# Kernel tuning notes

Measured on AMD Instinct MI355X. Metric: run time of the kernel, lower is better.

Reference implementation:

```python
import jax, jax.numpy as jnp
import numpy as np

B, S, D, H = 4, 1024, 1024, 16
DH = D // H


def setup_inputs() -> dict:
    key = jax.random.key(0)
    ks = jax.random.split(key, 9)
    s = 0.02
    return {
        "x": jax.random.normal(ks[0], (B, S, D), dtype=jnp.float32),
        "mask": jax.random.randint(ks[1], (B, 1, S), 0, 2, dtype=jnp.int32),
        "Wq": jax.random.normal(ks[2], (D, D), dtype=jnp.float32) * s,
        "bq": jnp.zeros((D,), dtype=jnp.float32),
        "Wk": jax.random.normal(ks[3], (D, D), dtype=jnp.float32) * s,
        "Wv": jax.random.normal(ks[4], (D, D), dtype=jnp.float32) * s,
        "bv": jnp.zeros((D,), dtype=jnp.float32),
        "Wo": jax.random.normal(ks[5], (D, D), dtype=jnp.float32) * s,
        "bo": jnp.zeros((D,), dtype=jnp.float32),
    }


def reference(x, mask, Wq, bq, Wk, Wv, bv, Wo, bo):
    # Linear projections (torch Linear: y = x @ W.T + b)
    q = x @ Wq.T + bq
    k = x @ Wk.T  # key has bias=False
    v = x @ Wv.T + bv

    scale = jnp.asarray(DH, x.dtype) ** (-0.25)
    # [B,S,D] -> [B,H,S,DH]
    qh = q.reshape(B, S, H, DH).transpose(0, 2, 1, 3) * scale
    kh = k.reshape(B, S, H, DH).transpose(0, 2, 1, 3) * scale
    vh = v.reshape(B, S, H, DH).transpose(0, 2, 1, 3)

    qk = jnp.einsum("bhqd,bhkd->bhqk", qh, kh)  # [B,H,S,S]

    # pad-mask branch: mask [B,1,S] -> [B,1,1,S], 0 means padded
    pad = (mask == 0)[:, :, None, :]
    min_value = jnp.finfo(qk.dtype).min
    qk = jnp.where(pad, min_value, qk)

    qk = qk.astype(jnp.float32)
    w = jax.nn.softmax(qk, axis=-1).astype(x.dtype)
    w = jnp.where(pad, jnp.asarray(0.0, w.dtype), w)

    wv = jnp.einsum("bhqk,bhkd->bhqd", w, vh)  # [B,H,S,DH]
    wv = wv.transpose(0, 2, 1, 3).reshape(B, S, D)
    out = wv @ Wo.T + bo
    return out, jax.lax.stop_gradient(qk)
```

## Files before the change

### kernel.cpp

```cpp
#include <hip/hip_runtime.h>

#define NB 4
#define NS 1024
#define ND 1024
#define NH 16
#define NDH 64

typedef __attribute__((ext_vector_type(8))) short short8;
typedef __attribute__((ext_vector_type(4))) short s16x4;
typedef __attribute__((ext_vector_type(4))) float f32x4;

#define SENT (-3.3895313892515355e38f)

static __device__ __forceinline__ unsigned short f2bf(float f) {
    unsigned u = __builtin_bit_cast(unsigned, f);
    u += 0x7fffu + ((u >> 16) & 1u);
    return (unsigned short)(u >> 16);
}

static __device__ __forceinline__ f32x4 mfma16(short8 a, short8 b, f32x4 c) {
    return __builtin_amdgcn_mfma_f32_16x16x32_bf16(a, b, c, 0, 0, 0);
}

typedef const __attribute__((address_space(1))) unsigned int gu32_t;
typedef __attribute__((address_space(3))) unsigned int su32_t;
#define GLOAD_LDS16(gp, lp) \
    __builtin_amdgcn_global_load_lds((gu32_t*)(const void*)(gp), (su32_t*)(void*)(lp), 16, 0, 0)

__global__ __launch_bounds__(256) void cast_to_bf16(
    const float* __restrict__ x,  const float* __restrict__ wq,
    const float* __restrict__ wk, const float* __restrict__ wv,
    const float* __restrict__ wo, short* __restrict__ xb,
    short* __restrict__ wqb, short* __restrict__ wkb,
    short* __restrict__ wvb, short* __restrict__ wob)
{
    int i = blockIdx.x * 256 + threadIdx.x;
    const float* s; short* d; int off;
    const int XQ = 1 << 20, WQ = 1 << 18;
    if (i < XQ)               { s = x;  d = xb;  off = i; }
    else if (i < XQ + WQ)     { s = wq; d = wqb; off = i - XQ; }
    else if (i < XQ + 2 * WQ) { s = wk; d = wkb; off = i - XQ - WQ; }
    else if (i < XQ + 3 * WQ) { s = wv; d = wvb; off = i - XQ - 2 * WQ; }
    else                      { s = wo; d = wob; off = i - XQ - 3 * WQ; }
    float4 v = ((const float4*)s)[off];
    s16x4 r = { (short)f2bf(v.x), (short)f2bf(v.y), (short)f2bf(v.z), (short)f2bf(v.w) };
    ((s16x4*)d)[off] = r;
}

__global__ __launch_bounds__(256) void gemm_bt_bf16(
    const short* __restrict__ X, const short* __restrict__ W,
    const float* __restrict__ bias, void* __restrict__ outp,
    float scale, int layout)
{
    __shared__ short As[128 * 64];
    __shared__ short Bs[128 * 64];
    const int tid = threadIdx.x;
    const int w = tid >> 6, l = tid & 63;
    const int lg = l >> 4, lc = l & 15;
    const int wr = w >> 1, wc = w & 1;
    const int bm = blockIdx.x, bn = blockIdx.y;
    const int K = ND;

    const f32x4 zf = {0.f, 0.f, 0.f, 0.f};
    f32x4 acc[4][4];
#pragma unroll
    for (int a = 0; a < 4; ++a)
#pragma unroll
        for (int b2 = 0; b2 < 4; ++b2) acc[a][b2] = zf;

    for (int t = 0; t < 16; ++t) {
        const int k0 = t * 64;
        __syncthreads();
#pragma unroll
        for (int i = 0; i < 4; ++i) {
            int lin = i * 256 + tid;
            int row = lin >> 3, cp = lin & 7;
            int c = cp ^ (row & 7);
            GLOAD_LDS16(X + (size_t)(bm * 128 + row) * K + k0 + c * 8, As + lin * 8);
            GLOAD_LDS16(W + (size_t)(bn * 128 + row) * K + k0 + c * 8, Bs + lin * 8);
        }
        __syncthreads();

        short8 af[4][2], bfr[4][2];
#pragma unroll
        for (int mb = 0; mb < 4; ++mb) {
            int r = wr * 64 + mb * 16 + lc;
#pragma unroll
            for (int ks = 0; ks < 2; ++ks) {
                int c = (ks * 4 + lg) ^ (r & 7);
                af[mb][ks] = *(const short8*)(As + r * 64 + c * 8);
            }
        }
#pragma unroll
        for (int nb = 0; nb < 4; ++nb) {
            int r = wc * 64 + nb * 16 + lc;
#pragma unroll
            for (int ks = 0; ks < 2; ++ks) {
                int c = (ks * 4 + lg) ^ (r & 7);
                bfr[nb][ks] = *(const short8*)(Bs + r * 64 + c * 8);
            }
        }
#pragma unroll
        for (int mb = 0; mb < 4; ++mb)
#pragma unroll
            for (int nb = 0; nb < 4; ++nb)
#pragma unroll
                for (int ks = 0; ks < 2; ++ks)
                    acc[mb][nb] = mfma16(af[mb][ks], bfr[nb][ks], acc[mb][nb]);
    }

#pragma unroll
    for (int mb = 0; mb < 4; ++mb) {
        int m0 = bm * 128 + wr * 64 + mb * 16 + lg * 4;
#pragma unroll
        for (int nb = 0; nb < 4; ++nb) {
            int n = bn * 128 + wc * 64 + nb * 16 + lc;
            float bv_ = bias ? bias[n] : 0.f;
#pragma unroll
            for (int r = 0; r < 4; ++r) {
                float v = (acc[mb][nb][r] + bv_) * scale;
                int mm = m0 + r;
                if (layout == 0) {
                    ((float*)outp)[(size_t)mm * ND + n] = v;
                } else {
                    int b = mm >> 10, s = mm & 1023, h = n >> 6, d = n & 63;
                    ((unsigned short*)outp)[(((size_t)(b * NH + h) * NS) + s) * NDH + d] = f2bf(v);
                }
            }
        }
    }
}

__global__ __launch_bounds__(256) void transpose_v(
    const unsigned short* __restrict__ vb, unsigned short* __restrict__ vt)
{
    __shared__ unsigned short T[64][65];
    const int st = blockIdx.x, bh = blockIdx.y;
    const int tid = threadIdx.x;
#pragma unroll
    for (int i = 0; i < 2; ++i) {
        int lin = i * 256 + tid;
        int s = lin >> 3, dc = (lin & 7) * 8;
        short8 v = *(const short8*)(vb + ((size_t)(bh * NS + st * 64 + s)) * NDH + dc);
#pragma unroll
        for (int e = 0; e < 8; ++e) T[s][dc + e] = (unsigned short)v[e];
    }
    __syncthreads();
#pragma unroll
    for (int i = 0; i < 2; ++i) {
        int lin = i * 256 + tid;
        int d = lin >> 3, sc = (lin & 7) * 8;
        short8 v;
#pragma unroll
        for (int e = 0; e < 8; ++e) v[e] = (short)T[sc + e][d];
        *(short8*)(vt + ((size_t)(bh * NDH + d)) * NS + st * 64 + sc) = v;
    }
}

__global__ __launch_bounds__(256) void attn_mfma(
    const short* __restrict__ qb, const short* __restrict__ kb,
    const short* __restrict__ vt, const int* __restrict__ mask,
    float* __restrict__ qk_out, unsigned short* __restrict__ wv_out)
{
    __shared__ short Ks[64 * 64];
    __shared__ short Vs[64 * 64];
    __shared__ short Ps[4][16 * 68];
    __shared__ int Msk[NS];
    const int qt = blockIdx.x, bh = blockIdx.y;
    const int b = bh >> 4, h = bh & 15;
    const int q0 = qt * 64;
    const int tid = threadIdx.x;
    const int w = tid >> 6, l = tid & 63;
    const int lg = l >> 4, lc = l & 15;

#pragma unroll
    for (int i = 0; i < 4; ++i) Msk[i * 256 + tid] = mask[b * NS + i * 256 + tid];

    short8 aq[2];
    {
        const short* qrow = qb + ((size_t)(bh * NS + q0 + w * 16 + lc)) * NDH;
#pragma unroll
        for (int ks = 0; ks < 2; ++ks) aq[ks] = *(const short8*)(qrow + ks * 32 + lg * 8);
    }

    const f32x4 zf = {0.f, 0.f, 0.f, 0.f};
    f32x4 o[4];
    float mr[4], lr[4];
#pragma unroll
    for (int r = 0; r < 4; ++r) { mr[r] = -INFINITY; lr[r] = 0.f; }
#pragma unroll
    for (int db = 0; db < 4; ++db) o[db] = zf;

    for (int t = 0; t < 16; ++t) {
        __syncthreads();
#pragma unroll
        for (int i = 0; i < 2; ++i) {
            int lin = i * 256 + tid;
            int row = lin >> 3, cp = lin & 7;
            int c = cp ^ (row & 7);
            GLOAD_LDS16(kb + ((size_t)(bh * NS + t * 64 + row)) * NDH + c * 8, Ks + lin * 8);
            GLOAD_LDS16(vt + ((size_t)(bh * NDH + row)) * NS + t * 64 + c * 8, Vs + lin * 8);
        }
        __syncthreads();

        f32x4 s[4];
#pragma unroll
        for (int jb = 0; jb < 4; ++jb) {
            s[jb] = zf;
#pragma unroll
            for (int ks = 0; ks < 2; ++ks) {
                int rk = jb * 16 + lc;
                int c = (ks * 4 + lg) ^ (rk & 7);
                short8 bk = *(const short8*)(Ks + rk * 64 + c * 8);
                s[jb] = mfma16(aq[ks], bk, s[jb]);
            }
        }

        int mj[4];
#pragma unroll
        for (int jb = 0; jb < 4; ++jb) mj[jb] = Msk[t * 64 + jb * 16 + lc];

        const size_t qrb = (size_t)(bh * NS + q0 + w * 16 + lg * 4) * NS + t * 64 + lc;
#pragma unroll
        for (int jb = 0; jb < 4; ++jb)
#pragma unroll
            for (int r = 0; r < 4; ++r)
                qk_out[qrb + (size_t)r * NS + jb * 16] = mj[jb] ? s[jb][r] : SENT;

        float tm[4];
#pragma unroll
        for (int r = 0; r < 4; ++r) {
            float a0 = mj[0] ? s[0][r] : -INFINITY;
            float a1 = mj[1] ? s[1][r] : -INFINITY;
            float a2 = mj[2] ? s[2][r] : -INFINITY;
            float a3 = mj[3] ? s[3][r] : -INFINITY;
            tm[r] = fmaxf(fmaxf(a0, a1), fmaxf(a2, a3));
        }
#pragma unroll
        for (int off = 1; off <= 8; off <<= 1)
#pragma unroll
            for (int r = 0; r < 4; ++r) tm[r] = fmaxf(tm[r], __shfl_xor(tm[r], off, 16));

        float f[4], nm[4];
#pragma unroll
        for (int r = 0; r < 4; ++r) {
            nm[r] = fmaxf(mr[r], tm[r]);
            f[r] = (nm[r] == -INFINITY) ? 1.f : __expf(mr[r] - nm[r]);
            mr[r] = nm[r];
        }
        float p[4][4], ts[4] = {0.f, 0.f, 0.f, 0.f};
#pragma unroll
        for (int jb = 0; jb < 4; ++jb)
#pragma unroll
            for (int r = 0; r < 4; ++r) {
                float e = mj[jb] ? __expf(s[jb][r] - nm[r]) : 0.f;
                p[jb][r] = e;
                ts[r] += e;
            }
#pragma unroll
        for (int off = 1; off <= 8; off <<= 1)
#pragma unroll
            for (int r = 0; r < 4; ++r) ts[r] += __shfl_xor(ts[r], off, 16);
        f32x4 fv = {f[0], f[1], f[2], f[3]};
#pragma unroll
        for (int r = 0; r < 4; ++r) lr[r] = lr[r] * f[r] + ts[r];
#pragma unroll
        for (int db = 0; db < 4; ++db) o[db] *= fv;

#pragma unroll
        for (int jb = 0; jb < 4; ++jb)
#pragma unroll
            for (int r = 0; r < 4; ++r)
                Ps[w][(lg * 4 + r) * 68 + jb * 16 + lc] = (short)f2bf(p[jb][r]);
        short8 pa[2];
#pragma unroll
        for (int ks = 0; ks < 2; ++ks)
            pa[ks] = *(const short8*)(&Ps[w][lc * 68 + ks * 32 + lg * 8]);

#pragma unroll
        for (int db = 0; db < 4; ++db)
#pragma unroll
            for (int ks = 0; ks < 2; ++ks) {
                int rv = db * 16 + lc;
                int c = (ks * 4 + lg) ^ (rv & 7);
                short8 bv = *(const short8*)(Vs + rv * 64 + c * 8);
                o[db] = mfma16(pa[ks], bv, o[db]);
            }
    }

    float inv[4];
#pragma unroll
    for (int r = 0; r < 4; ++r) inv[r] = (lr[r] > 0.f) ? 1.f / lr[r] : 0.f;
#pragma unroll
    for (int db = 0; db < 4; ++db)
#pragma unroll
        for (int r = 0; r < 4; ++r) {
            float v = o[db][r] * inv[r];
            wv_out[(((size_t)(b * NS + q0 + w * 16 + lg * 4 + r)) * NH + h) * NDH + db * 16 + lc] =
                f2bf(v);
        }
}

extern "C" void kernel_launch(void* const* d_in, const int* in_sizes, int n_in,
                              void* d_out, int out_size, void* d_ws, size_t ws_size,
                              hipStream_t stream) {
    const float* x    = (const float*)d_in[0];
    const int*   mask = (const int*)d_in[1];
    const float* Wq   = (const float*)d_in[2];
    const float* bq   = (const float*)d_in[3];
    const float* Wk   = (const float*)d_in[4];
    const float* Wv   = (const float*)d_in[5];
    const float* bv   = (const float*)d_in[6];
    const float* Wo   = (const float*)d_in[7];
    const float* bo   = (const float*)d_in[8];

    float* out    = (float*)d_out;
    float* qk_out = out + (size_t)NB * NS * ND;

    const size_t MI = 1u << 20;
    short* xb  = (short*)d_ws;
    short* wqb = xb  + 4 * MI;
    short* wkb = wqb + MI;
    short* wvb = wkb + MI;
    short* wob = wvb + MI;
    short* qbf = wob + MI;
    short* kbf = qbf + 4 * MI;
    short* vbf = kbf + 4 * MI;
    short* vtb = vbf + 4 * MI;
    short* wvo = vtb + 4 * MI;

    const float scale = 0.35355339059327373f;

    cast_to_bf16<<<8192, 256, 0, stream>>>(x, Wq, Wk, Wv, Wo, xb, wqb, wkb, wvb, wob);

    dim3 ggrid(32, 8), blk(256);
    gemm_bt_bf16<<<ggrid, blk, 0, stream>>>(xb, wqb, bq, qbf, scale, 1);
    gemm_bt_bf16<<<ggrid, blk, 0, stream>>>(xb, wkb, (const float*)nullptr, kbf, scale, 1);
    gemm_bt_bf16<<<ggrid, blk, 0, stream>>>(xb, wvb, bv, vbf, 1.0f, 1);

    dim3 tgrid(16, 64);
    transpose_v<<<tgrid, blk, 0, stream>>>((const unsigned short*)vbf, (unsigned short*)vtb);

    dim3 agrid(16, 64);
    attn_mfma<<<agrid, blk, 0, stream>>>(qbf, kbf, vtb, mask, qk_out, (unsigned short*)wvo);

    gemm_bt_bf16<<<ggrid, blk, 0, stream>>>(wvo, wob, bo, out, 1.0f, 0);
}
```

Baseline: 464.4 us.

## Batch QKV GEMMs into one launch and double-buffer K/V tiles in attention

The three Q/K/V projection GEMMs become a single launch that uses blockIdx.z to pick the weight, bias, scale and destination. This removes two launches and gives each wave of work three times as many blocks. The attention kernel now double-buffers its K/V shared-memory tiles, prefetching tile t+1 while computing on tile t, which drops one barrier per iteration. The output GEMM becomes its own kernel without the runtime layout branch. In exchange, attention shared-memory use doubles for K/V, which may lower occupancy.

```diff
diff --git a/kernel.cpp b/kernel.cpp
--- a/kernel.cpp
+++ b/kernel.cpp
@@ -47,10 +47,96 @@
     ((s16x4*)d)[off] = r;
 }
 
-__global__ __launch_bounds__(256) void gemm_bt_bf16(
+__global__ __launch_bounds__(256) void gemm_qkv(
+    const short* __restrict__ X, const short* __restrict__ Wq,
+    const short* __restrict__ Wk, const short* __restrict__ Wv,
+    const float* __restrict__ bq, const float* __restrict__ bv,
+    short* __restrict__ qd, short* __restrict__ kd, short* __restrict__ vd)
+{
+    __shared__ short As[128 * 64];
+    __shared__ short Bs[128 * 64];
+    const int z = blockIdx.z;
+    const short* W = (z == 0) ? Wq : (z == 1) ? Wk : Wv;
+    const float* bias = (z == 0) ? bq : (z == 1) ? (const float*)nullptr : bv;
+    const float scale = (z == 2) ? 1.0f : 0.35355339059327373f;
+    short* dst = (z == 0) ? qd : (z == 1) ? kd : vd;
+
+    const int tid = threadIdx.x;
+    const int w = tid >> 6, l = tid & 63;
+    const int lg = l >> 4, lc = l & 15;
+    const int wr = w >> 1, wc = w & 1;
+    const int bm = blockIdx.x, bn = blockIdx.y;
+    const int K = ND;
+
+    const f32x4 zf = {0.f, 0.f, 0.f, 0.f};
+    f32x4 acc[4][4];
+#pragma unroll
+    for (int a = 0; a < 4; ++a)
+#pragma unroll
+        for (int b2 = 0; b2 < 4; ++b2) acc[a][b2] = zf;
+
+    for (int t = 0; t < 16; ++t) {
+        const int k0 = t * 64;
+        __syncthreads();
+#pragma unroll
+        for (int i = 0; i < 4; ++i) {
+            int lin = i * 256 + tid;
+            int row = lin >> 3, cp = lin & 7;
+            int c = cp ^ (row & 7);
+            GLOAD_LDS16(X + (size_t)(bm * 128 + row) * K + k0 + c * 8, As + lin * 8);
+            GLOAD_LDS16(W + (size_t)(bn * 128 + row) * K + k0 + c * 8, Bs + lin * 8);
+        }
+        __syncthreads();
+
+        short8 af[4][2], bfr[4][2];
+#pragma unroll
+        for (int mb = 0; mb < 4; ++mb) {
+            int r = wr * 64 + mb * 16 + lc;
+#pragma unroll
+            for (int ks = 0; ks < 2; ++ks) {
+                int c = (ks * 4 + lg) ^ (r & 7);
+                af[mb][ks] = *(const short8*)(As + r * 64 + c * 8);
+            }
+        }
+#pragma unroll
+        for (int nb = 0; nb < 4; ++nb) {
+            int r = wc * 64 + nb * 16 + lc;
+#pragma unroll
+            for (int ks = 0; ks < 2; ++ks) {
+                int c = (ks * 4 + lg) ^ (r & 7);
+                bfr[nb][ks] = *(const short8*)(Bs + r * 64 + c * 8);
+            }
+        }
+#pragma unroll
+        for (int mb = 0; mb < 4; ++mb)
+#pragma unroll
+            for (int nb = 0; nb < 4; ++nb)
+#pragma unroll
+                for (int ks = 0; ks < 2; ++ks)
+                    acc[mb][nb] = mfma16(af[mb][ks], bfr[nb][ks], acc[mb][nb]);
+    }
+
+#pragma unroll
+    for (int mb = 0; mb < 4; ++mb) {
+        int m0 = bm * 128 + wr * 64 + mb * 16 + lg * 4;
+#pragma unroll
+        for (int nb = 0; nb < 4; ++nb) {
+            int n = bn * 128 + wc * 64 + nb * 16 + lc;
+            float bv_ = bias ? bias[n] : 0.f;
+#pragma unroll
+            for (int r = 0; r < 4; ++r) {
+                float v = (acc[mb][nb][r] + bv_) * scale;
+                int mm = m0 + r;
+                int b = mm >> 10, s = mm & 1023, h = n >> 6, d = n & 63;
+                ((unsigned short*)dst)[(((size_t)(b * NH + h) * NS) + s) * NDH + d] = f2bf(v);
+            }
+        }
+    }
+}
+
+__global__ __launch_bounds__(256) void gemm_out(
     const short* __restrict__ X, const short* __restrict__ W,
-    const float* __restrict__ bias, void* __restrict__ outp,
-    float scale, int layout)
+    const float* __restrict__ bias, float* __restrict__ outp)
 {
     __shared__ short As[128 * 64];
     __shared__ short Bs[128 * 64];
@@ -115,18 +201,10 @@
 #pragma unroll
         for (int nb = 0; nb < 4; ++nb) {
             int n = bn * 128 + wc * 64 + nb * 16 + lc;
-            float bv_ = bias ? bias[n] : 0.f;
-#pragma unroll
-            for (int r = 0; r < 4; ++r) {
-                float v = (acc[mb][nb][r] + bv_) * scale;
-                int mm = m0 + r;
-                if (layout == 0) {
-                    ((float*)outp)[(size_t)mm * ND + n] = v;
-                } else {
-                    int b = mm >> 10, s = mm & 1023, h = n >> 6, d = n & 63;
-                    ((unsigned short*)outp)[(((size_t)(b * NH + h) * NS) + s) * NDH + d] = f2bf(v);
-                }
-            }
+            float bv_ = bias[n];
+#pragma unroll
+            for (int r = 0; r < 4; ++r)
+                outp[(size_t)(m0 + r) * ND + n] = acc[mb][nb][r] + bv_;
         }
     }
 }
@@ -157,13 +235,27 @@
     }
 }
 
+static __device__ __forceinline__ void stage_kv(
+    const short* __restrict__ kb, const short* __restrict__ vt,
+    int bh, int t, int tid, short* Ksb, short* Vsb)
+{
+#pragma unroll
+    for (int i = 0; i < 2; ++i) {
+        int lin = i * 256 + tid;
+        int row = lin >> 3, cp = lin & 7;
+        int c = cp ^ (row & 7);
+        GLOAD_LDS16(kb + ((size_t)(bh * NS + t * 64 + row)) * NDH + c * 8, Ksb + lin * 8);
+        GLOAD_LDS16(vt + ((size_t)(bh * NDH + row)) * NS + t * 64 + c * 8, Vsb + lin * 8);
+    }
+}
+
 __global__ __launch_bounds__(256) void attn_mfma(
     const short* __restrict__ qb, const short* __restrict__ kb,
     const short* __restrict__ vt, const int* __restrict__ mask,
     float* __restrict__ qk_out, unsigned short* __restrict__ wv_out)
 {
-    __shared__ short Ks[64 * 64];
-    __shared__ short Vs[64 * 64];
+    __shared__ short Ks[2][64 * 64];
+    __shared__ short Vs[2][64 * 64];
     __shared__ short Ps[4][16 * 68];
     __shared__ int Msk[NS];
     const int qt = blockIdx.x, bh = blockIdx.y;
@@ -183,6 +275,8 @@
         for (int ks = 0; ks < 2; ++ks) aq[ks] = *(const short8*)(qrow + ks * 32 + lg * 8);
     }
 
+    stage_kv(kb, vt, bh, 0, tid, Ks[0], Vs[0]);
+
     const f32x4 zf = {0.f, 0.f, 0.f, 0.f};
     f32x4 o[4];
     float mr[4], lr[4];
@@ -191,17 +285,13 @@
 #pragma unroll
     for (int db = 0; db < 4; ++db) o[db] = zf;
 
+    __syncthreads();
+
     for (int t = 0; t < 16; ++t) {
-        __syncthreads();
-#pragma unroll
-        for (int i = 0; i < 2; ++i) {
-            int lin = i * 256 + tid;
-            int row = lin >> 3, cp = lin & 7;
-            int c = cp ^ (row & 7);
-            GLOAD_LDS16(kb + ((size_t)(bh * NS + t * 64 + row)) * NDH + c * 8, Ks + lin * 8);
-            GLOAD_LDS16(vt + ((size_t)(bh * NDH + row)) * NS + t * 64 + c * 8, Vs + lin * 8);
-        }
-        __syncthreads();
+        const int cur = t & 1;
+        if (t < 15) stage_kv(kb, vt, bh, t + 1, tid, Ks[cur ^ 1], Vs[cur ^ 1]);
+        const short* Ksc = Ks[cur];
+        const short* Vsc = Vs[cur];
 
         f32x4 s[4];
 #pragma unroll
@@ -211,7 +301,7 @@
             for (int ks = 0; ks < 2; ++ks) {
                 int rk = jb * 16 + lc;
                 int c = (ks * 4 + lg) ^ (rk & 7);
-                short8 bk = *(const short8*)(Ks + rk * 64 + c * 8);
+                short8 bk = *(const short8*)(Ksc + rk * 64 + c * 8);
                 s[jb] = mfma16(aq[ks], bk, s[jb]);
             }
         }
@@ -283,9 +373,11 @@
             for (int ks = 0; ks < 2; ++ks) {
                 int rv = db * 16 + lc;
                 int c = (ks * 4 + lg) ^ (rv & 7);
-                short8 bv = *(const short8*)(Vs + rv * 64 + c * 8);
+                short8 bv = *(const short8*)(Vsc + rv * 64 + c * 8);
                 o[db] = mfma16(pa[ks], bv, o[db]);
             }
+
+        __syncthreads();
     }
 
     float inv[4];
@@ -329,14 +421,11 @@
     short* vtb = vbf + 4 * MI;
     short* wvo = vtb + 4 * MI;
 
-    const float scale = 0.35355339059327373f;
-
     cast_to_bf16<<<8192, 256, 0, stream>>>(x, Wq, Wk, Wv, Wo, xb, wqb, wkb, wvb, wob);
 
-    dim3 ggrid(32, 8), blk(256);
-    gemm_bt_bf16<<<ggrid, blk, 0, stream>>>(xb, wqb, bq, qbf, scale, 1);
-    gemm_bt_bf16<<<ggrid, blk, 0, stream>>>(xb, wkb, (const float*)nullptr, kbf, scale, 1);
-    gemm_bt_bf16<<<ggrid, blk, 0, stream>>>(xb, wvb, bv, vbf, 1.0f, 1);
+    dim3 blk(256);
+    dim3 qgrid(32, 8, 3);
+    gemm_qkv<<<qgrid, blk, 0, stream>>>(xb, wqb, wkb, wvb, bq, bv, qbf, kbf, vbf);
 
     dim3 tgrid(16, 64);
     transpose_v<<<tgrid, blk, 0, stream>>>((const unsigned short*)vbf, (unsigned short*)vtb);
@@ -344,5 +433,6 @@
     dim3 agrid(16, 64);
     attn_mfma<<<agrid, blk, 0, stream>>>(qbf, kbf, vtb, mask, qk_out, (unsigned short*)wvo);
 
-    gemm_bt_bf16<<<ggrid, blk, 0, stream>>>(wvo, wob, bo, out, 1.0f, 0);
-}
+    dim3 ogrid(32, 8);
+    gemm_out<<<ogrid, blk, 0, stream>>>(wvo, wob, bo, out);
+}
```

Result: faster. 431.8 us (-7.0%).
